# Performance work log

Measured on AMD Instinct MI355X. Metric: run time of the kernel, lower is better.

## Reference

```python
import jax, jax.numpy as jnp
import numpy as np

D_MODEL = 128
N_LAYERS = 2
D_STATE = 16
D_CONV = 4
EXPAND = 2
GRID = 16
D_INNER = D_MODEL * EXPAND
DT_RANK = (D_MODEL + 15) // 16  # mamba_ssm default: ceil(d_model/16) = 8
BATCH = 128
SEQ = 200


def setup_inputs() -> dict:
    key = jax.random.key(0)
    ks = jax.random.split(key, 24)
    L = N_LAYERS

    def rn(k, shape, scale=0.02):
        return jax.random.normal(k, shape, dtype=jnp.float32) * scale

    A_init = jnp.log(jnp.broadcast_to(
        jnp.arange(1, D_STATE + 1, dtype=jnp.float32), (L, D_INNER, D_STATE)))
    kan_scale = 1.0 / (np.sqrt(D_MODEL) * np.sqrt(GRID))
    return {
        "x": jax.random.normal(ks[0], (BATCH, SEQ, D_MODEL), dtype=jnp.float32),
        "in_w": rn(ks[1], (L, 2 * D_INNER, D_MODEL)),
        "out_w": rn(ks[2], (L, D_MODEL, D_INNER)),
        "conv_w_f": rn(ks[3], (L, D_INNER, D_CONV), 0.1),
        "conv_b_f": rn(ks[4], (L, D_INNER), 0.01),
        "conv_w_b": rn(ks[5], (L, D_INNER, D_CONV), 0.1),
        "conv_b_b": rn(ks[6], (L, D_INNER), 0.01),
        "xproj_w_f": rn(ks[7], (L, DT_RANK + 2 * D_STATE, D_INNER)),
        "xproj_w_b": rn(ks[8], (L, DT_RANK + 2 * D_STATE, D_INNER)),
        "dtproj_w_f": rn(ks[9], (L, D_INNER, DT_RANK), 0.1),
        "dtproj_b_f": rn(ks[10], (L, D_INNER), 0.01),
        "dtproj_w_b": rn(ks[11], (L, D_INNER, DT_RANK), 0.1),
        "dtproj_b_b": rn(ks[12], (L, D_INNER), 0.01),
        "A_log_f": A_init,
        "A_log_b": A_init,
        "D_f": jnp.ones((L, D_INNER), jnp.float32),
        "D_b": jnp.ones((L, D_INNER), jnp.float32),
        "ln1_w": jnp.ones((L, D_MODEL), jnp.float32),
        "ln1_b": jnp.zeros((L, D_MODEL), jnp.float32),
        "ln_w": jnp.ones((L, D_MODEL), jnp.float32),
        "ln_b": jnp.zeros((L, D_MODEL), jnp.float32),
        "kan_coef": jax.random.normal(ks[13], (L, 2, D_MODEL, D_MODEL, GRID), dtype=jnp.float32) * kan_scale,
    }


def _ln(x, w, b, eps=1e-12):
    u = x.mean(-1, keepdims=True)
    s = ((x - u) ** 2).mean(-1, keepdims=True)
    return w * (x - u) / jnp.sqrt(s + eps) + b


def _silu(x):
    return x * jax.nn.sigmoid(x)


def _mamba(x, in_w, out_w, conv_w, conv_b, xp_w, dt_w, dt_b, A_log, Dp):
    # x: (B, L, d_model). Faithful to mamba_ssm Mamba (bias=False proj, conv_bias=True).
    B, L, _ = x.shape
    xz = jnp.einsum('bld,ed->ble', x, in_w)          # (B, L, 2*d_inner)
    xi, z = jnp.split(xz, 2, axis=-1)
    # causal depthwise conv over L
    xp = jnp.pad(xi, ((0, 0), (D_CONV - 1, 0), (0, 0)))
    xc = sum(xp[:, k:k + L, :] * conv_w[:, k] for k in range(D_CONV)) + conv_b
    xc = _silu(xc)                                    # (B, L, d_inner)
    dbl = jnp.einsum('ble,fe->blf', xc, xp_w)         # (B, L, dt_rank+2*d_state)
    dt = jax.nn.softplus(
        jnp.einsum('blr,dr->bld', dbl[..., :DT_RANK], dt_w) + dt_b)
    Bm = dbl[..., DT_RANK:DT_RANK + D_STATE]          # (B, L, d_state)
    Cm = dbl[..., DT_RANK + D_STATE:]
    A = -jnp.exp(A_log)                               # (d_inner, d_state)

    def step(h, inp):
        dt_t, u_t, b_t, c_t = inp                     # (B,di),(B,di),(B,ds),(B,ds)
        h = jnp.exp(dt_t[:, :, None] * A) * h + (dt_t * u_t)[:, :, None] * b_t[:, None, :]
        return h, jnp.einsum('bds,bs->bd', h, c_t)

    h0 = jnp.zeros((B, D_INNER, D_STATE), x.dtype)
    _, ys = jax.lax.scan(step, h0, (jnp.moveaxis(dt, 1, 0), jnp.moveaxis(xc, 1, 0),
                                    jnp.moveaxis(Bm, 1, 0), jnp.moveaxis(Cm, 1, 0)))
    y = jnp.moveaxis(ys, 0, 1) + xc * Dp              # (B, L, d_inner)
    y = y * _silu(z)
    return jnp.einsum('ble,de->bld', y, out_w)


def _kan(x, coef):
    # coef: (2, outdim, inputdim, grid)
    shp = x.shape
    xf = x.reshape(-1, shp[-1])                       # (N, d)
    kk = jnp.arange(1, GRID + 1, dtype=x.dtype)
    ang = xf[:, :, None] * kk                         # (N, d, grid)
    y = (jnp.einsum('nig,jig->nj', jnp.cos(ang), coef[0])
         + jnp.einsum('nig,jig->nj', jnp.sin(ang), coef[1]))
    return y.reshape(shp[:-1] + (coef.shape[1],))


def reference(x, in_w, out_w, conv_w_f, conv_b_f, conv_w_b, conv_b_b,
              xproj_w_f, xproj_w_b, dtproj_w_f, dtproj_b_f, dtproj_w_b, dtproj_b_b,
              A_log_f, A_log_b, D_f, D_b, ln1_w, ln1_b, ln_w, ln_b, kan_coef):
    feats = []
    h = x
    for l in range(N_LAYERS):
        o = _ln(h, ln1_w[l], ln1_b[l])
        f = _mamba(o, in_w[l], out_w[l], conv_w_f[l], conv_b_f[l],
                   xproj_w_f[l], dtproj_w_f[l], dtproj_b_f[l], A_log_f[l], D_f[l])
        b = _mamba(o[:, ::-1], in_w[l], out_w[l], conv_w_b[l], conv_b_b[l],
                   xproj_w_b[l], dtproj_w_b[l], dtproj_b_b[l], A_log_b[l], D_b[l])[:, ::-1]
        o = _ln(f + b, ln_w[l], ln_b[l])
        o = _kan(o, kan_coef[l])  # dropout p=0.0 (eval) -> identity
        h = o + h
        feats.append(h)
    return sum(feats) / len(feats)
```

## Files before the change

kernel.cpp:

```cpp
#include <hip/hip_runtime.h>
#include <hip/hip_bf16.h>
#include <cmath>

#define BATCH 128
#define SEQ 200
#define DMODEL 128
#define DINNER 256
#define DSTATE 16
#define NTOK (BATCH * SEQ)

typedef __bf16 bf16x8 __attribute__((ext_vector_type(8)));
typedef float f32x4 __attribute__((ext_vector_type(4)));

__device__ __forceinline__ unsigned short f2bf(float f) {
  union { float f; unsigned u; } x{f};
  const unsigned r = x.u + 0x7fffu + ((x.u >> 16) & 1u);
  return (unsigned short)(r >> 16);
}
__device__ __forceinline__ float bf2f(unsigned short h) {
  union { unsigned u; float f; } x{(unsigned)h << 16};
  return x.f;
}
__device__ __forceinline__ void split2(float a, float b, unsigned& hp, unsigned& lp) {
  const unsigned short ha = f2bf(a), hb = f2bf(b);
  const float ra = a - bf2f(ha), rb = b - bf2f(hb);
  hp = (unsigned)ha | ((unsigned)hb << 16);
  lp = (unsigned)f2bf(ra) | ((unsigned)f2bf(rb) << 16);
}

template <int CTRL>
__device__ __forceinline__ float dpp_add(float v) {
  const int r = __builtin_amdgcn_update_dpp(0, __float_as_int(v), CTRL, 0xF, 0xF, true);
  return v + __int_as_float(r);
}

__device__ __forceinline__ float silu_f(float x) {
  return x / (1.f + __expf(-x));
}

__global__ __launch_bounds__(256) void ln_stats(const float* __restrict__ in,
                                                float* __restrict__ st) {
  const int wv = threadIdx.x >> 6;
  const int lane = threadIdx.x & 63;
  const int row = blockIdx.x * 4 + wv;
  const float2 v = *(const float2*)(in + (size_t)row * DMODEL + lane * 2);
  float s = v.x + v.y;
#pragma unroll
  for (int o = 32; o; o >>= 1) s += __shfl_xor(s, o, 64);
  const float u = s * (1.f / 128.f);
  const float dx = v.x - u, dy = v.y - u;
  float sq = dx * dx + dy * dy;
#pragma unroll
  for (int o = 32; o; o >>= 1) sq += __shfl_xor(sq, o, 64);
  const float inv = rsqrtf(sq * (1.f / 128.f) + 1e-12f);
  if (lane == 0) *(float2*)(st + 2 * (size_t)row) = make_float2(u, inv);
}

__global__ __launch_bounds__(256) void wprep(const float* __restrict__ in_w,
                                             const float* __restrict__ xpwf,
                                             const float* __restrict__ xpwb,
                                             const float* __restrict__ out_w,
                                             unsigned short* __restrict__ iwH,
                                             unsigned short* __restrict__ iwL,
                                             unsigned short* __restrict__ xfH,
                                             unsigned short* __restrict__ xfL,
                                             unsigned short* __restrict__ xbH,
                                             unsigned short* __restrict__ xbL,
                                             unsigned short* __restrict__ owH,
                                             unsigned short* __restrict__ owL) {
  const int idx = blockIdx.x * 256 + threadIdx.x;
  float w;
  unsigned short *H, *L;
  int off;
  if (idx < 65536)      { w = in_w[idx];        H = iwH; L = iwL; off = idx; }
  else if (idx < 75776) { w = xpwf[idx - 65536]; H = xfH; L = xfL; off = idx - 65536; }
  else if (idx < 86016) { w = xpwb[idx - 75776]; H = xbH; L = xbL; off = idx - 75776; }
  else                  { w = out_w[idx - 86016]; H = owH; L = owL; off = idx - 86016; }
  const unsigned short h = f2bf(w);
  H[off] = h;
  L[off] = f2bf(w - bf2f(h));
}

template <int MODE>
__global__ __launch_bounds__(256) void gemm_c(const float* __restrict__ A1,
                                              const float* __restrict__ A2,
                                              const float* __restrict__ stats,
                                              const float* __restrict__ lw,
                                              const float* __restrict__ lb,
                                              const unsigned short* __restrict__ Whi,
                                              const unsigned short* __restrict__ Wlo,
                                              float* __restrict__ C,
                                              const unsigned short* __restrict__ Whi2,
                                              const unsigned short* __restrict__ Wlo2,
                                              float* __restrict__ C2,
                                              int M, int N, int K) {
  __shared__ unsigned short AshH[64 * 40], AshL[64 * 40];
  __shared__ unsigned short BshH[128 * 40], BshL[128 * 40];
  const float* Ause = A1;
  const unsigned short* WH = Whi;
  const unsigned short* WL = Wlo;
  float* Cuse = C;
  if (MODE == 2 && blockIdx.z == 1) { Ause = A2; WH = Whi2; WL = Wlo2; Cuse = C2; }
  const int tid = threadIdx.x;
  const int m0 = blockIdx.y * 64;
  const int n0 = blockIdx.x * 128;
  const int lane = tid & 63;
  const int wid = tid >> 6;
  const int arow = lane & 15;
  const int kch = (lane >> 4) * 8;
  const int bcol = wid * 32 + (lane & 15);
  f32x4 acc[4][2] = {};
  for (int k0 = 0; k0 < K; k0 += 32) {
    __syncthreads();
    {
      const int row = tid >> 2;
      const int koff = (tid & 3) * 8;
      const int m = m0 + row;
      float4 v0 = *(const float4*)(Ause + (size_t)m * K + k0 + koff);
      float4 v1 = *(const float4*)(Ause + (size_t)m * K + k0 + koff + 4);
      if (MODE == 1) {
        const float2 st = *(const float2*)(stats + 2 * (size_t)m);
        const float4 w0 = *(const float4*)(lw + k0 + koff);
        const float4 w1 = *(const float4*)(lw + k0 + koff + 4);
        const float4 b0 = *(const float4*)(lb + k0 + koff);
        const float4 b1 = *(const float4*)(lb + k0 + koff + 4);
        v0.x = fmaf(w0.x, (v0.x - st.x) * st.y, b0.x);
        v0.y = fmaf(w0.y, (v0.y - st.x) * st.y, b0.y);
        v0.z = fmaf(w0.z, (v0.z - st.x) * st.y, b0.z);
        v0.w = fmaf(w0.w, (v0.w - st.x) * st.y, b0.w);
        v1.x = fmaf(w1.x, (v1.x - st.x) * st.y, b1.x);
        v1.y = fmaf(w1.y, (v1.y - st.x) * st.y, b1.y);
        v1.z = fmaf(w1.z, (v1.z - st.x) * st.y, b1.z);
        v1.w = fmaf(w1.w, (v1.w - st.x) * st.y, b1.w);
      }
      unsigned h0, l0, h1, l1, h2, l2, h3, l3;
      split2(v0.x, v0.y, h0, l0);
      split2(v0.z, v0.w, h1, l1);
      split2(v1.x, v1.y, h2, l2);
      split2(v1.z, v1.w, h3, l3);
      *(uint4*)&AshH[row * 40 + koff] = make_uint4(h0, h1, h2, h3);
      *(uint4*)&AshL[row * 40 + koff] = make_uint4(l0, l1, l2, l3);
    }
    {
      const int row = tid >> 1;
      const int koff = (tid & 1) * 16;
      const int n = n0 + row;
      uint4 wh0 = make_uint4(0, 0, 0, 0), wh1 = wh0, wl0 = wh0, wl1 = wh0;
      if (n < N) {
        wh0 = *(const uint4*)(WH + (size_t)n * K + k0 + koff);
        wh1 = *(const uint4*)(WH + (size_t)n * K + k0 + koff + 8);
        wl0 = *(const uint4*)(WL + (size_t)n * K + k0 + koff);
        wl1 = *(const uint4*)(WL + (size_t)n * K + k0 + koff + 8);
      }
      *(uint4*)&BshH[row * 40 + koff] = wh0;
      *(uint4*)&BshH[row * 40 + koff + 8] = wh1;
      *(uint4*)&BshL[row * 40 + koff] = wl0;
      *(uint4*)&BshL[row * 40 + koff + 8] = wl1;
    }
    __syncthreads();
    const bf16x8 bh0 = *(const bf16x8*)&BshH[bcol * 40 + kch];
    const bf16x8 bh1 = *(const bf16x8*)&BshH[(bcol + 16) * 40 + kch];
    const bf16x8 bl0 = *(const bf16x8*)&BshL[bcol * 40 + kch];
    const bf16x8 bl1 = *(const bf16x8*)&BshL[(bcol + 16) * 40 + kch];
#pragma unroll
    for (int g = 0; g < 4; ++g) {
      const bf16x8 ah = *(const bf16x8*)&AshH[(g * 16 + arow) * 40 + kch];
      const bf16x8 al = *(const bf16x8*)&AshL[(g * 16 + arow) * 40 + kch];
      acc[g][0] = __builtin_amdgcn_mfma_f32_16x16x32_bf16(ah, bh0, acc[g][0], 0, 0, 0);
      acc[g][0] = __builtin_amdgcn_mfma_f32_16x16x32_bf16(al, bh0, acc[g][0], 0, 0, 0);
      acc[g][0] = __builtin_amdgcn_mfma_f32_16x16x32_bf16(ah, bl0, acc[g][0], 0, 0, 0);
      acc[g][1] = __builtin_amdgcn_mfma_f32_16x16x32_bf16(ah, bh1, acc[g][1], 0, 0, 0);
      acc[g][1] = __builtin_amdgcn_mfma_f32_16x16x32_bf16(al, bh1, acc[g][1], 0, 0, 0);
      acc[g][1] = __builtin_amdgcn_mfma_f32_16x16x32_bf16(ah, bl1, acc[g][1], 0, 0, 0);
    }
  }
  const int q0 = (lane >> 4) * 4;
#pragma unroll
  for (int g = 0; g < 4; ++g)
#pragma unroll
    for (int fc = 0; fc < 2; ++fc)
#pragma unroll
      for (int q = 0; q < 4; ++q) {
        const int m = m0 + g * 16 + q0 + q;
        const int n = n0 + wid * 32 + fc * 16 + (lane & 15);
        if (n < N) Cuse[(size_t)m * N + n] = acc[g][fc][q];
      }
}

__global__ __launch_bounds__(256) void gemm_oln(const float* __restrict__ A1,
                                                const float* __restrict__ A2v,
                                                const float* __restrict__ Zp,
                                                const unsigned short* __restrict__ Whi,
                                                const unsigned short* __restrict__ Wlo,
                                                const float* __restrict__ lw,
                                                const float* __restrict__ lb,
                                                float* __restrict__ o2out) {
  __shared__ unsigned short AshH[64 * 40], AshL[64 * 40];
  __shared__ unsigned short BshH[128 * 40], BshL[128 * 40];
  __shared__ float Csh[64][132];
  const int tid = threadIdx.x;
  const int m0 = blockIdx.x * 64;
  const int lane = tid & 63;
  const int wid = tid >> 6;
  const int arow = lane & 15;
  const int kch = (lane >> 4) * 8;
  const int bcol = wid * 32 + (lane & 15);
  f32x4 acc[4][2] = {};
  for (int k0 = 0; k0 < 256; k0 += 32) {
    __syncthreads();
    {
      const int row = tid >> 2;
      const int koff = (tid & 3) * 8;
      const int m = m0 + row;
      float4 v0 = *(const float4*)(A1 + (size_t)m * 256 + k0 + koff);
      float4 v1 = *(const float4*)(A1 + (size_t)m * 256 + k0 + koff + 4);
      const float4 u0 = *(const float4*)(A2v + (size_t)m * 256 + k0 + koff);
      const float4 u1 = *(const float4*)(A2v + (size_t)m * 256 + k0 + koff + 4);
      const float4 z0 = *(const float4*)(Zp + (size_t)m * 512 + k0 + koff);
      const float4 z1 = *(const float4*)(Zp + (size_t)m * 512 + k0 + koff + 4);
      v0.x = (v0.x + u0.x) * silu_f(z0.x);
      v0.y = (v0.y + u0.y) * silu_f(z0.y);
      v0.z = (v0.z + u0.z) * silu_f(z0.z);
      v0.w = (v0.w + u0.w) * silu_f(z0.w);
      v1.x = (v1.x + u1.x) * silu_f(z1.x);
      v1.y = (v1.y + u1.y) * silu_f(z1.y);
      v1.z = (v1.z + u1.z) * silu_f(z1.z);
      v1.w = (v1.w + u1.w) * silu_f(z1.w);
      unsigned h0, l0, h1, l1, h2, l2, h3, l3;
      split2(v0.x, v0.y, h0, l0);
      split2(v0.z, v0.w, h1, l1);
      split2(v1.x, v1.y, h2, l2);
      split2(v1.z, v1.w, h3, l3);
      *(uint4*)&AshH[row * 40 + koff] = make_uint4(h0, h1, h2, h3);
      *(uint4*)&AshL[row * 40 + koff] = make_uint4(l0, l1, l2, l3);
    }
    {
      const int row = tid >> 1;
      const int koff = (tid & 1) * 16;
      const uint4 wh0 = *(const uint4*)(Whi + (size_t)row * 256 + k0 + koff);
      const uint4 wh1 = *(const uint4*)(Whi + (size_t)row * 256 + k0 + koff + 8);
      const uint4 wl0 = *(const uint4*)(Wlo + (size_t)row * 256 + k0 + koff);
      const uint4 wl1 = *(const uint4*)(Wlo + (size_t)row * 256 + k0 + koff + 8);
      *(uint4*)&BshH[row * 40 + koff] = wh0;
      *(uint4*)&BshH[row * 40 + koff + 8] = wh1;
      *(uint4*)&BshL[row * 40 + koff] = wl0;
      *(uint4*)&BshL[row * 40 + koff + 8] = wl1;
    }
    __syncthreads();
    const bf16x8 bh0 = *(const bf16x8*)&BshH[bcol * 40 + kch];
    const bf16x8 bh1 = *(const bf16x8*)&BshH[(bcol + 16) * 40 + kch];
    const bf16x8 bl0 = *(const bf16x8*)&BshL[bcol * 40 + kch];
    const bf16x8 bl1 = *(const bf16x8*)&BshL[(bcol + 16) * 40 + kch];
#pragma unroll
    for (int g = 0; g < 4; ++g) {
      const bf16x8 ah = *(const bf16x8*)&AshH[(g * 16 + arow) * 40 + kch];
      const bf16x8 al = *(const bf16x8*)&AshL[(g * 16 + arow) * 40 + kch];
      acc[g][0] = __builtin_amdgcn_mfma_f32_16x16x32_bf16(ah, bh0, acc[g][0], 0, 0, 0);
      acc[g][0] = __builtin_amdgcn_mfma_f32_16x16x32_bf16(al, bh0, acc[g][0], 0, 0, 0);
      acc[g][0] = __builtin_amdgcn_mfma_f32_16x16x32_bf16(ah, bl0, acc[g][0], 0, 0, 0);
      acc[g][1] = __builtin_amdgcn_mfma_f32_16x16x32_bf16(ah, bh1, acc[g][1], 0, 0, 0);
      acc[g][1] = __builtin_amdgcn_mfma_f32_16x16x32_bf16(al, bh1, acc[g][1], 0, 0, 0);
      acc[g][1] = __builtin_amdgcn_mfma_f32_16x16x32_bf16(ah, bl1, acc[g][1], 0, 0, 0);
    }
  }
  __syncthreads();
  const int q0 = (lane >> 4) * 4;
#pragma unroll
  for (int g = 0; g < 4; ++g)
#pragma unroll
    for (int fc = 0; fc < 2; ++fc)
#pragma unroll
      for (int q = 0; q < 4; ++q)
        Csh[g * 16 + q0 + q][wid * 32 + fc * 16 + (lane & 15)] = acc[g][fc][q];
  __syncthreads();
  const int row = tid >> 2;
  const int c0 = (tid & 3) * 32;
  float vloc[32];
  float s = 0.f;
#pragma unroll
  for (int j = 0; j < 32; ++j) {
    vloc[j] = Csh[row][c0 + j];
    s += vloc[j];
  }
  s = dpp_add<0xB1>(s);
  s = dpp_add<0x4E>(s);
  const float u = s * (1.f / 128.f);
  float sq = 0.f;
#pragma unroll
  for (int j = 0; j < 32; ++j) {
    const float dd = vloc[j] - u;
    sq += dd * dd;
  }
  sq = dpp_add<0xB1>(sq);
  sq = dpp_add<0x4E>(sq);
  const float inv = rsqrtf(sq * (1.f / 128.f) + 1e-12f);
  float* outp = o2out + (size_t)(m0 + row) * 128 + c0;
#pragma unroll
  for (int j4 = 0; j4 < 8; ++j4) {
    const float4 wv = *(const float4*)(lw + c0 + j4 * 4);
    const float4 bv = *(const float4*)(lb + c0 + j4 * 4);
    float4 o;
    o.x = fmaf(wv.x, (vloc[j4 * 4 + 0] - u) * inv, bv.x);
    o.y = fmaf(wv.y, (vloc[j4 * 4 + 1] - u) * inv, bv.y);
    o.z = fmaf(wv.z, (vloc[j4 * 4 + 2] - u) * inv, bv.z);
    o.w = fmaf(wv.w, (vloc[j4 * 4 + 3] - u) * inv, bv.w);
    *(float4*)(outp + j4 * 4) = o;
  }
}

__global__ __launch_bounds__(256) void conv_silu_kernel(const float* __restrict__ xz,
                                                        const float* __restrict__ cwf,
                                                        const float* __restrict__ cbf,
                                                        const float* __restrict__ cwb,
                                                        const float* __restrict__ cbb,
                                                        float* __restrict__ xcf,
                                                        float* __restrict__ xcb) {
  const int n0 = blockIdx.x * 8;
  const int l0 = n0 % SEQ;
  const int e = threadIdx.x;
  const float4 wf = *(const float4*)(cwf + e * 4);
  const float4 wb = *(const float4*)(cwb + e * 4);
  const float bfv = cbf[e], bbv = cbb[e];
  const float* px = xz + (size_t)n0 * 512 + e;
  float w[7];
#pragma unroll
  for (int j = 0; j < 6; ++j) {
    const int l = l0 - 3 + j;
    w[j] = (l >= 0 && l < SEQ) ? px[(j - 3) * 512] : 0.f;
  }
#pragma unroll
  for (int t = 0; t < 8; ++t) {
    const int l = l0 + t;
    w[6] = (l + 3 < SEQ) ? px[(t + 3) * 512] : 0.f;
    const float af = fmaf(wf.x, w[0], fmaf(wf.y, w[1], fmaf(wf.z, w[2], fmaf(wf.w, w[3], bfv))));
    const float ab = fmaf(wb.x, w[6], fmaf(wb.y, w[5], fmaf(wb.z, w[4], fmaf(wb.w, w[3], bbv))));
    xcf[(size_t)(n0 + t) * DINNER + e] = silu_f(af);
    xcb[(size_t)(n0 + t) * DINNER + e] = silu_f(ab);
#pragma unroll
    for (int j = 0; j < 6; ++j) w[j] = w[j + 1];
  }
}

__global__ __launch_bounds__(256) void dtsp_kernel2(const float* __restrict__ dblF,
                                                    const float* __restrict__ dblB,
                                                    const float* __restrict__ dtwF,
                                                    const float* __restrict__ dtbF,
                                                    const float* __restrict__ dtwB,
                                                    const float* __restrict__ dtbB,
                                                    float* __restrict__ dtF,
                                                    float* __restrict__ dtB) {
  const int bwd = blockIdx.y;
  const float* __restrict__ dbl = bwd ? dblB : dblF;
  const float* __restrict__ dtw = bwd ? dtwB : dtwF;
  const float* __restrict__ dtb = bwd ? dtbB : dtbF;
  float* __restrict__ dt = bwd ? dtB : dtF;
  __shared__ float r[8][8];
  const int n0 = blockIdx.x * 8;
  const int d = threadIdx.x;
  if (threadIdx.x < 64) {
    const int tt = threadIdx.x >> 3, j = threadIdx.x & 7;
    r[tt][j] = dbl[(size_t)(n0 + tt) * 40 + j];
  }
  const float4 w0 = *(const float4*)(dtw + d * 8);
  const float4 w1 = *(const float4*)(dtw + d * 8 + 4);
  const float bd = dtb[d];
  __syncthreads();
#pragma unroll
  for (int tt = 0; tt < 8; ++tt) {
    float acc = bd;
    acc += r[tt][0] * w0.x + r[tt][1] * w0.y + r[tt][2] * w0.z + r[tt][3] * w0.w;
    acc += r[tt][4] * w1.x + r[tt][5] * w1.y + r[tt][6] * w1.z + r[tt][7] * w1.w;
    const float sp = acc > 20.f ? acc : log1pf(__expf(acc));
    dt[(size_t)(n0 + tt) * DINNER + d] = sp;
  }
}

template <int SX, int SB>
__device__ __forceinline__ void scan_body(const float* __restrict__ dt,
                                          float* __restrict__ xc,
                                          const float* __restrict__ dbl,
                                          const float* __restrict__ Alog,
                                          const float* __restrict__ Dp,
                                          int bb) {
  const int lane = threadIdx.x & 63;
  const int wid = threadIdx.x >> 6;
  const int q = lane & 3;
  const int dl = lane >> 2;
  const int d = blockIdx.x * 64 + wid * 16 + dl;
  const float LOG2E = 1.44269504f;
  const float4 al = *(const float4*)(Alog + d * DSTATE + q * 4);
  const float4 A2 = make_float4(-__expf(al.x) * LOG2E, -__expf(al.y) * LOG2E,
                                -__expf(al.z) * LOG2E, -__expf(al.w) * LOG2E);
  const float Dd = Dp[d];
  const int t0 = (SX > 0) ? 0 : (SEQ - 1);
  int offX = (bb * SEQ + t0) * DINNER + d;
  int offB = (bb * SEQ + t0) * 40 + 8 + q * 4;
  float4 h = make_float4(0.f, 0.f, 0.f, 0.f);

  float adt[4], au[4]; float4 aB[4], aC[4];
  float bdt[4], bu[4]; float4 bB[4], bC[4];

  auto loadg = [&](float* gdt, float* gu, float4* gB, float4* gC, int oX, int oB) {
#pragma unroll
    for (int k = 0; k < 4; ++k) {
      gdt[k] = dt[oX + k * SX];
      gu[k] = xc[oX + k * SX];
      gB[k] = *(const float4*)(dbl + oB + k * SB);
      gC[k] = *(const float4*)(dbl + oB + k * SB + 16);
    }
  };
  auto computeg = [&](const float* gdt, const float* gu, const float4* gB,
                      const float4* gC, int oX) {
#pragma unroll
    for (int k = 0; k < 4; ++k) {
      const float dtv = gdt[k];
      const float u = gu[k];
      const float du = dtv * u;
      float4 a;
      a.x = exp2f(dtv * A2.x);
      a.y = exp2f(dtv * A2.y);
      a.z = exp2f(dtv * A2.z);
      a.w = exp2f(dtv * A2.w);
      h.x = fmaf(a.x, h.x, du * gB[k].x);
      h.y = fmaf(a.y, h.y, du * gB[k].y);
      h.z = fmaf(a.z, h.z, du * gB[k].z);
      h.w = fmaf(a.w, h.w, du * gB[k].w);
      float pp = fmaf(h.w, gC[k].w, fmaf(h.z, gC[k].z, fmaf(h.y, gC[k].y, h.x * gC[k].x)));
      pp = dpp_add<0xB1>(pp);
      pp = dpp_add<0x4E>(pp);
      if (q == 0) xc[oX + k * SX] = fmaf(u, Dd, pp);
    }
  };

  loadg(adt, au, aB, aC, offX, offB);
  for (int t = 0; t < SEQ; t += 8) {
    loadg(bdt, bu, bB, bC, offX + 4 * SX, offB + 4 * SB);
    computeg(adt, au, aB, aC, offX);
    if (t + 8 < SEQ) loadg(adt, au, aB, aC, offX + 8 * SX, offB + 8 * SB);
    computeg(bdt, bu, bB, bC, offX + 4 * SX);
    offX += 8 * SX;
    offB += 8 * SB;
  }
}

__global__ __launch_bounds__(256, 4) void scan_kernel5(
    const float* __restrict__ dtF, float* xcF, const float* __restrict__ dblF,
    const float* __restrict__ AlogF, const float* __restrict__ DF,
    const float* __restrict__ dtB, float* xcB, const float* __restrict__ dblB,
    const float* __restrict__ AlogB, const float* __restrict__ DB) {
  if (blockIdx.z == 0)
    scan_body<DINNER, 40>(dtF, xcF, dblF, AlogF, DF, blockIdx.y);
  else
    scan_body<-DINNER, -40>(dtB, xcB, dblB, AlogB, DB, blockIdx.y);
}

__global__ __launch_bounds__(256) void kan_prep(const float* __restrict__ coef,
                                                unsigned short* __restrict__ Wt) {
  const int idx = blockIdx.x * 256 + threadIdx.x;
  const int k = idx & 31;
  const int j = (idx >> 5) & 127;
  const int i = idx >> 12;
  const int c = k >> 4, g = k & 15;
  Wt[idx] = f2bf(coef[(((size_t)c * 128 + j) * 128 + i) * 16 + g]);
}

__global__ __launch_bounds__(256) void kan_mfma(const float* __restrict__ x,
                                                const unsigned short* __restrict__ Wt,
                                                const float* __restrict__ hin,
                                                float* __restrict__ hout,
                                                float* __restrict__ accum,
                                                int first) {
  __shared__ float Xs[128 * 64];
  __shared__ unsigned short F[2][64 * 40];
  __shared__ unsigned short Wsh[2][128 * 40];
  const int tid = threadIdx.x;
  const int n0 = blockIdx.x * 64;
  const int wid = tid >> 6;
  const int lane = tid & 63;
  {
    const int tok = tid & 63;
    const int cq = tid >> 6;
#pragma unroll
    for (int r = 0; r < 8; ++r) {
      const int i0 = cq * 32 + r * 4;
      const float4 v = *(const float4*)(x + (size_t)(n0 + tok) * 128 + i0);
      Xs[(i0 + 0) * 64 + tok] = v.x;
      Xs[(i0 + 1) * 64 + tok] = v.y;
      Xs[(i0 + 2) * 64 + tok] = v.z;
      Xs[(i0 + 3) * 64 + tok] = v.w;
    }
  }
  const int fs = tid >> 7;
  const int fn = (tid & 127) >> 1;
  const int fh = tid & 1;
  const int wrow = tid & 127;
  const int arow = lane & 15;
  const int kch = (lane >> 4) * 8;
  const int bcol = wid * 32 + (lane & 15);
  f32x4 acc[4][2] = {};
  for (int ii = 0; ii < 128; ii += 2) {
    __syncthreads();
    {
      const uint4* src = (const uint4*)(Wt + (size_t)(ii + fs) * 4096 + wrow * 32);
      uint4* dst = (uint4*)&Wsh[fs][wrow * 40];
      dst[0] = src[0]; dst[1] = src[1]; dst[2] = src[2]; dst[3] = src[3];
    }
    {
      const float xv = Xs[(ii + fs) * 64 + fn];
      const float c1 = __cosf(xv), s1 = __sinf(xv);
      float c, s;
      if (fh == 0) { c = c1; s = s1; }
      else {
        const float y = xv * 9.f;
        c = __cosf(y); s = __sinf(y);
      }
      unsigned int* Fu = (unsigned int*)F[fs];
#pragma unroll
      for (int p = 0; p < 4; ++p) {
        const float c2 = c * c1 - s * s1;
        const float s2 = s * c1 + c * s1;
        Fu[fn * 20 + fh * 4 + p]     = (unsigned)f2bf(c) | ((unsigned)f2bf(c2) << 16);
        Fu[fn * 20 + 8 + fh * 4 + p] = (unsigned)f2bf(s) | ((unsigned)f2bf(s2) << 16);
        c = c2 * c1 - s2 * s1;
        s = s2 * c1 + c2 * s1;
      }
    }
    __syncthreads();
#pragma unroll
    for (int sl = 0; sl < 2; ++sl) {
      const bf16x8 b0 = *(const bf16x8*)&Wsh[sl][bcol * 40 + kch];
      const bf16x8 b1 = *(const bf16x8*)&Wsh[sl][(bcol + 16) * 40 + kch];
#pragma unroll
      for (int g = 0; g < 4; ++g) {
        const bf16x8 a = *(const bf16x8*)&F[sl][(g * 16 + arow) * 40 + kch];
        acc[g][0] = __builtin_amdgcn_mfma_f32_16x16x32_bf16(a, b0, acc[g][0], 0, 0, 0);
        acc[g][1] = __builtin_amdgcn_mfma_f32_16x16x32_bf16(a, b1, acc[g][1], 0, 0, 0);
      }
    }
  }
  const int q0 = (lane >> 4) * 4;
#pragma unroll
  for (int g = 0; g < 4; ++g)
#pragma unroll
    for (int fc = 0; fc < 2; ++fc)
#pragma unroll
      for (int q = 0; q < 4; ++q) {
        const int n = n0 + g * 16 + q0 + q;
        const int j = wid * 32 + fc * 16 + (lane & 15);
        const size_t off = (size_t)n * 128 + j;
        const float v = acc[g][fc][q] + hin[off];
        hout[off] = v;
        const float a = 0.5f * v;
        accum[off] = first ? a : (accum[off] + a);
      }
}

extern "C" void kernel_launch(void* const* d_in, const int* in_sizes, int n_in,
                              void* d_out, int out_size, void* d_ws, size_t ws_size,
                              hipStream_t stream) {
  (void)in_sizes; (void)n_in; (void)out_size;
  const float* x     = (const float*)d_in[0];
  const float* in_w  = (const float*)d_in[1];
  const float* out_w = (const float*)d_in[2];
  const float* cwf   = (const float*)d_in[3];
  const float* cbf   = (const float*)d_in[4];
  const float* cwb   = (const float*)d_in[5];
  const float* cbb   = (const float*)d_in[6];
  const float* xpwf  = (const float*)d_in[7];
  const float* xpwb  = (const float*)d_in[8];
  const float* dtwf  = (const float*)d_in[9];
  const float* dtbf  = (const float*)d_in[10];
  const float* dtwb  = (const float*)d_in[11];
  const float* dtbb  = (const float*)d_in[12];
  const float* Alogf = (const float*)d_in[13];
  const float* Alogb = (const float*)d_in[14];
  const float* Dfp   = (const float*)d_in[15];
  const float* Dbp   = (const float*)d_in[16];
  const float* ln1w  = (const float*)d_in[17];
  const float* ln1b  = (const float*)d_in[18];
  const float* lnw   = (const float*)d_in[19];
  const float* lnb   = (const float*)d_in[20];
  const float* kanc  = (const float*)d_in[21];
  float* outp = (float*)d_out;

  int C = 128;
  while (C > 8) {
    const size_t need = ((size_t)761856 + (size_t)2000 * C * SEQ) * 4;
    if (need <= ws_size) break;
    C >>= 1;
  }
  const int T = C * SEQ;

  unsigned short* usbase = (unsigned short*)d_ws;
  unsigned short* Wt_l[2];
  unsigned short *iwH[2], *iwL[2], *xfH[2], *xfL[2], *xbH[2], *xbL[2], *owH[2], *owL[2];
  for (int l = 0; l < 2; ++l) {
    Wt_l[l] = usbase + (size_t)l * 524288;
    unsigned short* q = usbase + 2 * 524288 + (size_t)l * 237568;
    iwH[l] = q;           iwL[l] = q + 65536;
    xfH[l] = q + 131072;  xfL[l] = q + 141312;
    xbH[l] = q + 151552;  xbL[l] = q + 161792;
    owH[l] = q + 172032;  owL[l] = q + 204800;
  }
  float* pf = (float*)d_ws + 761856;
  float* stats = pf; pf += (size_t)T * 2;
  float* xzb  = pf; pf += (size_t)T * 512;
  float* xcf  = pf; pf += (size_t)T * 256;
  float* xcb  = pf; pf += (size_t)T * 256;
  float* dblf = pf; pf += (size_t)T * 40;
  float* dblb = pf; pf += (size_t)T * 40;
  float* dtf  = pf; pf += (size_t)T * 256;
  float* dtb  = pf; pf += (size_t)T * 256;
  float* o2   = pf; pf += (size_t)T * 128;
  float* hbuf = pf; pf += (size_t)T * 128;

  for (int l = 0; l < 2; ++l) {
    wprep<<<464, 256, 0, stream>>>(in_w + (size_t)l * 65536, xpwf + (size_t)l * 10240,
                                   xpwb + (size_t)l * 10240, out_w + (size_t)l * 32768,
                                   iwH[l], iwL[l], xfH[l], xfL[l],
                                   xbH[l], xbL[l], owH[l], owL[l]);
    kan_prep<<<2048, 256, 0, stream>>>(kanc + (size_t)l * 2 * 128 * 128 * 16, Wt_l[l]);
  }

  for (int b0 = 0; b0 < BATCH; b0 += C) {
    const size_t tok0 = (size_t)b0 * SEQ;
    for (int l = 0; l < 2; ++l) {
      const float* hin = (l == 0) ? (x + tok0 * 128) : hbuf;
      ln_stats<<<T / 4, 256, 0, stream>>>(hin, stats);
      gemm_c<1><<<dim3(4, T / 64), 256, 0, stream>>>(
          hin, (const float*)nullptr, stats, ln1w + l * 128, ln1b + l * 128,
          iwH[l], iwL[l], xzb,
          (const unsigned short*)nullptr, (const unsigned short*)nullptr,
          (float*)nullptr, T, 512, 128);
      conv_silu_kernel<<<T / 8, 256, 0, stream>>>(xzb, cwf + l * 1024, cbf + l * 256,
                                                  cwb + l * 1024, cbb + l * 256, xcf, xcb);
      gemm_c<2><<<dim3(1, T / 64, 2), 256, 0, stream>>>(
          xcf, xcb, (const float*)nullptr, (const float*)nullptr, (const float*)nullptr,
          xfH[l], xfL[l], dblf, xbH[l], xbL[l], dblb, T, 40, 256);
      dtsp_kernel2<<<dim3(T / 8, 2), 256, 0, stream>>>(dblf, dblb,
                                                       dtwf + l * 2048, dtbf + l * 256,
                                                       dtwb + l * 2048, dtbb + l * 256,
                                                       dtf, dtb);
      scan_kernel5<<<dim3(4, C, 2), 256, 0, stream>>>(
          dtf, xcf, dblf, Alogf + l * 4096, Dfp + l * 256,
          dtb, xcb, dblb, Alogb + l * 4096, Dbp + l * 256);
      gemm_oln<<<T / 64, 256, 0, stream>>>(xcf, xcb, xzb + 256, owH[l], owL[l],
                                           lnw + l * 128, lnb + l * 128, o2);
      kan_mfma<<<T / 64, 256, 0, stream>>>(o2, Wt_l[l], hin, hbuf,
                                           outp + tok0 * 128, l == 0 ? 1 : 0);
    }
  }
}
```

Before: 616.0 us.

## Store LN output transposed so KAN kernel reads features directly from global

The out-projection+LayerNorm kernel now writes its output in feature-major (transposed) layout, and the KAN MFMA kernel drops its 32KB shared-memory staging/transposition buffer and reads each feature column straight from global memory inside the loop. This is meant to cut LDS usage (raising occupancy) and remove the upfront transpose. In exchange, gemm_oln's stores become scalar and strided across rows, although consecutive rows in a wavefront still coalesce. KAN now issues a global load on every iteration, adding latency to the inner loop.

```diff
diff --git a/kernel.cpp b/kernel.cpp
--- a/kernel.cpp
+++ b/kernel.cpp
@@ -194,7 +194,8 @@
                                                 const unsigned short* __restrict__ Wlo,
                                                 const float* __restrict__ lw,
                                                 const float* __restrict__ lb,
-                                                float* __restrict__ o2out) {
+                                                float* __restrict__ o2T,
+                                                int Ttot) {
   __shared__ unsigned short AshH[64 * 40], AshL[64 * 40];
   __shared__ unsigned short BshH[128 * 40], BshL[128 * 40];
   __shared__ float Csh[64][132];
@@ -294,17 +295,12 @@
   sq = dpp_add<0xB1>(sq);
   sq = dpp_add<0x4E>(sq);
   const float inv = rsqrtf(sq * (1.f / 128.f) + 1e-12f);
-  float* outp = o2out + (size_t)(m0 + row) * 128 + c0;
-#pragma unroll
-  for (int j4 = 0; j4 < 8; ++j4) {
-    const float4 wv = *(const float4*)(lw + c0 + j4 * 4);
-    const float4 bv = *(const float4*)(lb + c0 + j4 * 4);
-    float4 o;
-    o.x = fmaf(wv.x, (vloc[j4 * 4 + 0] - u) * inv, bv.x);
-    o.y = fmaf(wv.y, (vloc[j4 * 4 + 1] - u) * inv, bv.y);
-    o.z = fmaf(wv.z, (vloc[j4 * 4 + 2] - u) * inv, bv.z);
-    o.w = fmaf(wv.w, (vloc[j4 * 4 + 3] - u) * inv, bv.w);
-    *(float4*)(outp + j4 * 4) = o;
+  const int m = m0 + row;
+#pragma unroll
+  for (int j = 0; j < 32; ++j) {
+    const float wv = lw[c0 + j];
+    const float bv = lb[c0 + j];
+    o2T[(size_t)(c0 + j) * Ttot + m] = fmaf(wv, (vloc[j] - u) * inv, bv);
   }
 }
 
@@ -464,32 +460,19 @@
   Wt[idx] = f2bf(coef[(((size_t)c * 128 + j) * 128 + i) * 16 + g]);
 }
 
-__global__ __launch_bounds__(256) void kan_mfma(const float* __restrict__ x,
+__global__ __launch_bounds__(256) void kan_mfma(const float* __restrict__ xT,
+                                                int Ttot,
                                                 const unsigned short* __restrict__ Wt,
                                                 const float* __restrict__ hin,
                                                 float* __restrict__ hout,
                                                 float* __restrict__ accum,
                                                 int first) {
-  __shared__ float Xs[128 * 64];
   __shared__ unsigned short F[2][64 * 40];
   __shared__ unsigned short Wsh[2][128 * 40];
   const int tid = threadIdx.x;
   const int n0 = blockIdx.x * 64;
   const int wid = tid >> 6;
   const int lane = tid & 63;
-  {
-    const int tok = tid & 63;
-    const int cq = tid >> 6;
-#pragma unroll
-    for (int r = 0; r < 8; ++r) {
-      const int i0 = cq * 32 + r * 4;
-      const float4 v = *(const float4*)(x + (size_t)(n0 + tok) * 128 + i0);
-      Xs[(i0 + 0) * 64 + tok] = v.x;
-      Xs[(i0 + 1) * 64 + tok] = v.y;
-      Xs[(i0 + 2) * 64 + tok] = v.z;
-      Xs[(i0 + 3) * 64 + tok] = v.w;
-    }
-  }
   const int fs = tid >> 7;
   const int fn = (tid & 127) >> 1;
   const int fh = tid & 1;
@@ -497,6 +480,7 @@
   const int arow = lane & 15;
   const int kch = (lane >> 4) * 8;
   const int bcol = wid * 32 + (lane & 15);
+  const float* xcol = xT + (size_t)fs * Ttot + n0 + fn;
   f32x4 acc[4][2] = {};
   for (int ii = 0; ii < 128; ii += 2) {
     __syncthreads();
@@ -506,7 +490,7 @@
       dst[0] = src[0]; dst[1] = src[1]; dst[2] = src[2]; dst[3] = src[3];
     }
     {
-      const float xv = Xs[(ii + fs) * 64 + fn];
+      const float xv = xcol[(size_t)ii * Ttot];
       const float c1 = __cosf(xv), s1 = __sinf(xv);
       float c, s;
       if (fh == 0) { c = c1; s = s1; }
@@ -611,7 +595,7 @@
   float* dblb = pf; pf += (size_t)T * 40;
   float* dtf  = pf; pf += (size_t)T * 256;
   float* dtb  = pf; pf += (size_t)T * 256;
-  float* o2   = pf; pf += (size_t)T * 128;
+  float* o2T  = pf; pf += (size_t)T * 128;
   float* hbuf = pf; pf += (size_t)T * 128;
 
   for (int l = 0; l < 2; ++l) {
@@ -645,8 +629,8 @@
           dtf, xcf, dblf, Alogf + l * 4096, Dfp + l * 256,
           dtb, xcb, dblb, Alogb + l * 4096, Dbp + l * 256);
       gemm_oln<<<T / 64, 256, 0, stream>>>(xcf, xcb, xzb + 256, owH[l], owL[l],
-                                           lnw + l * 128, lnb + l * 128, o2);
-      kan_mfma<<<T / 64, 256, 0, stream>>>(o2, Wt_l[l], hin, hbuf,
+                                           lnw + l * 128, lnb + l * 128, o2T, T);
+      kan_mfma<<<T / 64, 256, 0, stream>>>(o2T, T, Wt_l[l], hin, hbuf,
                                            outp + tok0 * 128, l == 0 ? 1 : 0);
     }
   }
```

Result: slower. 631.6 us (+2.5%).
